# Kernel tuning notes

Hardware: AMD Instinct MI355X
Metric: run time of the kernel (lower is better)

The kernel has to match this reference:

```python
import jax, jax.numpy as jnp
import numpy as np


def maxpool2x2(x):
    # NCHW 2x2 max pool, stride 2
    return jax.lax.reduce_window(x, -jnp.inf, jax.lax.max, (1, 1, 2, 2), (1, 1, 2, 2), 'VALID')


def _xavier_uniform(k, shape):
    fan_out, fan_in = shape
    lim = np.sqrt(6.0 / (fan_in + fan_out))
    return jax.random.uniform(k, shape, jnp.float32, -lim, lim)


def setup_inputs() -> dict:
    key = jax.random.key(0)
    ks = jax.random.split(key, 5)
    C = 64
    x = jax.random.normal(ks[0], (4, C, 128, 128), jnp.float32)
    Wq = _xavier_uniform(ks[1], (C // 8, C))  # 1x1 conv == channel matmul
    Wk = _xavier_uniform(ks[2], (C // 8, C))
    Wv = _xavier_uniform(ks[3], (C // 2, C))
    Wo = _xavier_uniform(ks[4], (C, C // 2))
    gamma = jnp.full((1,), 0.1, jnp.float32)  # nonzero so attention branch contributes
    return {"x": x, "Wq": Wq, "Wk": Wk, "Wv": Wv, "Wo": Wo, "gamma": gamma}


def reference(x, Wq, Wk, Wv, Wo, gamma):
    b, c, w, h = x.shape
    # 1x1 convs as channel contractions
    q = jnp.einsum('oc,bchw->bohw', Wq, x).reshape(b, c // 8, w * h)          # [b, c/8, k]
    k_ = maxpool2x2(jnp.einsum('oc,bchw->bohw', Wk, x)).reshape(b, c // 8, -1)  # [b, c/8, f]
    v = maxpool2x2(jnp.einsum('oc,bchw->bohw', Wv, x)).reshape(b, c // 2, -1)   # [b, c/2, f]
    # softmax over full-resolution query positions k (last axis), per pooled position f
    weights = jax.nn.softmax(jnp.einsum('bcf,bck->bfk', k_, q), axis=-1)        # [b, f, k]
    out = jnp.einsum('bcf,bfk->bck', v, weights).reshape(b, c // 2, w, h)       # [b, c/2, w, h]
    out = jnp.einsum('oc,bchw->bohw', Wo, out)                                   # [b, c, w, h]
    return gamma * out + x
```

## Files before the change

### kernel.cpp

```cpp
#include <hip/hip_runtime.h>
#include <cstdint>
#include <cstddef>


#define LOG2E 1.44269504088896340736f

typedef __attribute__((ext_vector_type(8)))  __bf16 bf8_t;
typedef __attribute__((ext_vector_type(16))) float  fx16;

__device__ __forceinline__ unsigned short f2bf(float f) {
  unsigned int u = __builtin_bit_cast(unsigned int, f);
  u += 0x7FFFu + ((u >> 16) & 1u);
  return (unsigned short)(u >> 16);
}
__device__ __forceinline__ unsigned int pk2(unsigned short lo, unsigned short hi) {
  return (unsigned int)lo | ((unsigned int)hi << 16);
}
__device__ __forceinline__ int pi16(int s) {
  int m = (s >> 2) & 3;
  return (m == 1 || m == 2) ? (s ^ 12) : s;
}
__device__ __forceinline__ float max4(const float* a) {
  return fmaxf(fmaxf(a[0], a[1]), fmaxf(a[2], a[3]));
}

#if __has_builtin(__builtin_amdgcn_exp2f)
#define EXP2F __builtin_amdgcn_exp2f
#else
#define EXP2F exp2f
#endif

__global__ void __launch_bounds__(256) k_qkv(const float* __restrict__ x,
                                             const float* __restrict__ Wq,
                                             const float* __restrict__ Wk,
                                             const float* __restrict__ Wv,
                                             const float* __restrict__ Wo,
                                             unsigned short* __restrict__ Qp,
                                             unsigned short* __restrict__ KpB,
                                             float* __restrict__ Vp,
                                             unsigned short* __restrict__ Wop) {
  if (blockIdx.x == 256) {
    for (int i = threadIdx.x; i < 2048; i += 256) {
      int c = i & 31;
      Wop[i] = f2bf(Wo[(i & ~31) | (c & 16) | pi16(c & 15)]);
    }
    return;
  }
  __shared__ float ws[48][64];
  __shared__ float xs[16][256];
  int t = threadIdx.x;
  for (int i = t; i < 512; i += 256) {
    ws[i >> 6][i & 63] = Wq[i];
    ws[8 + (i >> 6)][i & 63] = Wk[i];
  }
  for (int i = t; i < 2048; i += 256) ws[16 + (i >> 6)][i & 63] = Wv[i];
  int b = blockIdx.x >> 6, frow = blockIdx.x & 63;
  int rg = t >> 6, fc = t & 63;
  const float* xb = x + (size_t)b * (64 * 16384) + frow * 256;
  float acc[12][4];
#pragma unroll
  for (int j = 0; j < 12; ++j)
#pragma unroll
    for (int p = 0; p < 4; ++p) acc[j][p] = 0.f;
  int cl = t >> 4, seg = t & 15;
  for (int cc = 0; cc < 4; ++cc) {
    __syncthreads();
    const float4* src =
        reinterpret_cast<const float4*>(xb + (size_t)(cc * 16 + cl) * 16384 + seg * 16);
    float4* dst = reinterpret_cast<float4*>(&xs[cl][seg * 16]);
#pragma unroll
    for (int j = 0; j < 4; ++j) dst[j] = src[j];
    __syncthreads();
#pragma unroll
    for (int c16 = 0; c16 < 16; ++c16) {
      int c = cc * 16 + c16;
      float2 xa = *reinterpret_cast<const float2*>(&xs[c16][2 * fc]);
      float2 xbv = *reinterpret_cast<const float2*>(&xs[c16][128 + 2 * fc]);
#pragma unroll
      for (int j = 0; j < 12; ++j) {
        float w = ws[12 * rg + j][c];
        acc[j][0] = fmaf(w, xa.x, acc[j][0]);
        acc[j][1] = fmaf(w, xa.y, acc[j][1]);
        acc[j][2] = fmaf(w, xbv.x, acc[j][2]);
        acc[j][3] = fmaf(w, xbv.y, acc[j][3]);
      }
    }
  }
  size_t idx = (size_t)b * 4096 + frow * 64 + fc;
  uint4 z4; z4.x = z4.y = z4.z = z4.w = 0u;
  if (rg == 0) {
#pragma unroll
    for (int p = 0; p < 4; ++p) {
      int kpos = frow * 256 + (p >> 1) * 128 + 2 * fc + (p & 1);
      uint4 qa;
      qa.x = pk2(f2bf(acc[0][p]), f2bf(acc[1][p]));
      qa.y = pk2(f2bf(acc[2][p]), f2bf(acc[3][p]));
      qa.z = pk2(f2bf(acc[4][p]), f2bf(acc[5][p]));
      qa.w = pk2(f2bf(acc[6][p]), f2bf(acc[7][p]));
      uint4* qdst = reinterpret_cast<uint4*>(Qp + ((size_t)b * 16384 + kpos) * 16);
      qdst[0] = qa; qdst[1] = z4;
    }
    uint2 kw;
    kw.x = pk2(f2bf(max4(acc[8]) * LOG2E), f2bf(max4(acc[9]) * LOG2E));
    kw.y = pk2(f2bf(max4(acc[10]) * LOG2E), f2bf(max4(acc[11]) * LOG2E));
    *reinterpret_cast<uint2*>(KpB + idx * 16) = kw;
  } else if (rg == 1) {
    uint2 kw;
    kw.x = pk2(f2bf(max4(acc[0]) * LOG2E), f2bf(max4(acc[1]) * LOG2E));
    kw.y = pk2(f2bf(max4(acc[2]) * LOG2E), f2bf(max4(acc[3]) * LOG2E));
    *reinterpret_cast<uint2*>(KpB + idx * 16 + 4) = kw;
    *reinterpret_cast<uint4*>(KpB + idx * 16 + 8) = z4;
    float* vd = Vp + idx * 32;
    *reinterpret_cast<float4*>(vd) =
        make_float4(max4(acc[4]), max4(acc[5]), max4(acc[6]), max4(acc[7]));
    *reinterpret_cast<float4*>(vd + 4) =
        make_float4(max4(acc[8]), max4(acc[9]), max4(acc[10]), max4(acc[11]));
  } else {
    float* vd = Vp + idx * 32 + (rg == 2 ? 8 : 20);
#pragma unroll
    for (int j4 = 0; j4 < 3; ++j4)
      *reinterpret_cast<float4*>(vd + 4 * j4) =
          make_float4(max4(acc[4 * j4]), max4(acc[4 * j4 + 1]),
                      max4(acc[4 * j4 + 2]), max4(acc[4 * j4 + 3]));
  }
}

__global__ void __launch_bounds__(1024) k_lsum(const unsigned short* __restrict__ Qp,
                                               const unsigned short* __restrict__ KpB,
                                               const float* __restrict__ Vp,
                                               unsigned short* __restrict__ Vpp) {
  int b = blockIdx.x >> 6, g = blockIdx.x & 63;
  int wv = threadIdx.x >> 6, lane = threadIdx.x & 63;
  int half = lane >> 5, l31 = lane & 31;
  const unsigned short* kb =
      KpB + ((size_t)(b * 4096 + g * 64 + l31)) * 16 + half * 8;
  bf8_t A0 = *reinterpret_cast<const bf8_t*>(kb);
  bf8_t A1 = *reinterpret_cast<const bf8_t*>(kb + 32 * 16);
  const unsigned short* qbase = Qp + ((size_t)b * 16384) * 16 + half * 8;
  fx16 z;
#pragma unroll
  for (int i = 0; i < 16; ++i) z[i] = 0.f;
  float l[32];
#pragma unroll
  for (int i = 0; i < 32; ++i) l[i] = 0.f;
  int t0 = wv * 32;
  bf8_t B = *reinterpret_cast<const bf8_t*>(qbase + (size_t)(t0 * 32 + l31) * 16);
  for (int i = 0; i < 32; ++i) {
    int tn = t0 + ((i + 1) & 31);
    bf8_t nB = *reinterpret_cast<const bf8_t*>(qbase + (size_t)(tn * 32 + l31) * 16);
    fx16 s0 = __builtin_amdgcn_mfma_f32_32x32x16_bf16(A0, B, z, 0, 0, 0);
    fx16 s1 = __builtin_amdgcn_mfma_f32_32x32x16_bf16(A1, B, z, 0, 0, 0);
#pragma unroll
    for (int r0 = 0; r0 < 16; ++r0) l[r0] += EXP2F(s0[r0]);
#pragma unroll
    for (int r0 = 0; r0 < 16; ++r0) l[16 + r0] += EXP2F(s1[r0]);
    B = nB;
  }
#pragma unroll
  for (int r0 = 0; r0 < 32; ++r0)
    for (int d = 1; d < 32; d <<= 1) l[r0] += __shfl_xor(l[r0], d);
  __shared__ float sl[16][2][32];
  __shared__ float Linv[64];
  __shared__ unsigned short Tv[32][72];
  if (l31 == 0) {
#pragma unroll
    for (int r0 = 0; r0 < 16; ++r0) {
      int row = (r0 & 3) + 8 * (r0 >> 2) + 4 * half;
      sl[wv][0][row] = l[r0];
      sl[wv][1][row] = l[16 + r0];
    }
  }
  __syncthreads();
  if (threadIdx.x < 64) {
    int fgi = threadIdx.x >> 5, row = threadIdx.x & 31;
    float L = 0.f;
#pragma unroll
    for (int w2 = 0; w2 < 16; ++w2) L += sl[w2][fgi][row];
    Linv[threadIdx.x] = 1.0f / L;
  }
  __syncthreads();
  if (threadIdx.x < 512) {
    int floc = threadIdx.x >> 3, c4 = (threadIdx.x & 7) * 4;
    float4 v = *reinterpret_cast<const float4*>(
        Vp + ((size_t)(b * 4096 + g * 64 + floc)) * 32 + c4);
    float s = Linv[floc];
    int dst = (floc & ~15) | pi16(floc & 15);
    Tv[c4][dst]     = f2bf(v.x * s);
    Tv[c4 + 1][dst] = f2bf(v.y * s);
    Tv[c4 + 2][dst] = f2bf(v.z * s);
    Tv[c4 + 3][dst] = f2bf(v.w * s);
  }
  __syncthreads();
  if (threadIdx.x < 256) {
    int c = threadIdx.x >> 3, u = threadIdx.x & 7;
    uint4 val = *reinterpret_cast<const uint4*>(&Tv[c][u * 8]);
    *reinterpret_cast<uint4*>(Vpp + ((size_t)(b * 32 + c)) * 4096 + g * 64 + u * 8) = val;
  }
}

__global__ void __launch_bounds__(512) k_attn(const unsigned short* __restrict__ Qp,
                                              const unsigned short* __restrict__ KpB,
                                              const unsigned short* __restrict__ Vpp,
                                              const unsigned short* __restrict__ Wop,
                                              const float* __restrict__ x,
                                              const float* __restrict__ gamma,
                                              float* __restrict__ out) {
  int b = blockIdx.x >> 8, kp = blockIdx.x & 255;
  int wv = threadIdx.x >> 6, lane = threadIdx.x & 63;
  int half = lane >> 5, l31 = lane & 31;
  int kbase = kp * 64;
  const unsigned short* qb = Qp + ((size_t)b * 16384 + kbase + l31) * 16 + half * 8;
  bf8_t Bq0 = *reinterpret_cast<const bf8_t*>(qb);
  bf8_t Bq1 = *reinterpret_cast<const bf8_t*>(qb + 32 * 16);
  fx16 z;
#pragma unroll
  for (int i = 0; i < 16; ++i) z[i] = 0.f;
  fx16 acc0 = z, acc1 = z;
  const unsigned short* kpB = KpB + ((size_t)b * 4096 + l31) * 16 + half * 8;
  const unsigned short* vpB = Vpp + ((size_t)(b * 32 + l31)) * 4096 + half * 8;
  int c0 = wv * 16;
  int f0 = c0 * 32;
  bf8_t Ak  = *reinterpret_cast<const bf8_t*>(kpB + (size_t)f0 * 16);
  bf8_t Av0 = *reinterpret_cast<const bf8_t*>(vpB + f0);
  bf8_t Av1 = *reinterpret_cast<const bf8_t*>(vpB + f0 + 16);
  for (int fc = 0; fc < 16; ++fc) {
    int f1 = (c0 + ((fc + 1) & 15)) * 32;
    bf8_t nAk  = *reinterpret_cast<const bf8_t*>(kpB + (size_t)f1 * 16);
    bf8_t nAv0 = *reinterpret_cast<const bf8_t*>(vpB + f1);
    bf8_t nAv1 = *reinterpret_cast<const bf8_t*>(vpB + f1 + 16);
    fx16 s0 = __builtin_amdgcn_mfma_f32_32x32x16_bf16(Ak, Bq0, z, 0, 0, 0);
    fx16 s1 = __builtin_amdgcn_mfma_f32_32x32x16_bf16(Ak, Bq1, z, 0, 0, 0);
    bf8_t P00, P01, P10, P11;
#pragma unroll
    for (int j = 0; j < 8; ++j) {
      P00[j] = (__bf16)EXP2F(s0[j]);
      P01[j] = (__bf16)EXP2F(s0[8 + j]);
    }
#pragma unroll
    for (int j = 0; j < 8; ++j) {
      P10[j] = (__bf16)EXP2F(s1[j]);
      P11[j] = (__bf16)EXP2F(s1[8 + j]);
    }
    acc0 = __builtin_amdgcn_mfma_f32_32x32x16_bf16(Av0, P00, acc0, 0, 0, 0);
    acc1 = __builtin_amdgcn_mfma_f32_32x32x16_bf16(Av0, P10, acc1, 0, 0, 0);
    acc0 = __builtin_amdgcn_mfma_f32_32x32x16_bf16(Av1, P01, acc0, 0, 0, 0);
    acc1 = __builtin_amdgcn_mfma_f32_32x32x16_bf16(Av1, P11, acc1, 0, 0, 0);
    Ak = nAk; Av0 = nAv0; Av1 = nAv1;
  }
  __shared__ float sacc[4][2][4][64][4];
  if (wv >= 4) {
    int s = wv - 4;
#pragma unroll
    for (int j4 = 0; j4 < 4; ++j4) {
      *reinterpret_cast<float4*>(&sacc[s][0][j4][lane][0]) =
          make_float4(acc0[4 * j4], acc0[4 * j4 + 1], acc0[4 * j4 + 2], acc0[4 * j4 + 3]);
      *reinterpret_cast<float4*>(&sacc[s][1][j4][lane][0]) =
          make_float4(acc1[4 * j4], acc1[4 * j4 + 1], acc1[4 * j4 + 2], acc1[4 * j4 + 3]);
    }
  }
  __syncthreads();
  if (wv < 4) {
#pragma unroll
    for (int j4 = 0; j4 < 4; ++j4) {
      float4 p0 = *reinterpret_cast<const float4*>(&sacc[wv][0][j4][lane][0]);
      float4 p1 = *reinterpret_cast<const float4*>(&sacc[wv][1][j4][lane][0]);
      p0.x += acc0[4 * j4]; p0.y += acc0[4 * j4 + 1];
      p0.z += acc0[4 * j4 + 2]; p0.w += acc0[4 * j4 + 3];
      p1.x += acc1[4 * j4]; p1.y += acc1[4 * j4 + 1];
      p1.z += acc1[4 * j4 + 2]; p1.w += acc1[4 * j4 + 3];
      *reinterpret_cast<float4*>(&sacc[wv][0][j4][lane][0]) = p0;
      *reinterpret_cast<float4*>(&sacc[wv][1][j4][lane][0]) = p1;
    }
  }
  __syncthreads();
  if (wv >= 4) return;
  int kt = wv & 1, ot = wv >> 1;
  fx16 tot;
#pragma unroll
  for (int j4 = 0; j4 < 4; ++j4) {
    float4 a0 = *reinterpret_cast<const float4*>(&sacc[0][kt][j4][lane][0]);
    float4 a1 = *reinterpret_cast<const float4*>(&sacc[1][kt][j4][lane][0]);
    float4 a2 = *reinterpret_cast<const float4*>(&sacc[2][kt][j4][lane][0]);
    float4 a3 = *reinterpret_cast<const float4*>(&sacc[3][kt][j4][lane][0]);
    tot[4 * j4]     = (a0.x + a1.x) + (a2.x + a3.x);
    tot[4 * j4 + 1] = (a0.y + a1.y) + (a2.y + a3.y);
    tot[4 * j4 + 2] = (a0.z + a1.z) + (a2.z + a3.z);
    tot[4 * j4 + 3] = (a0.w + a1.w) + (a2.w + a3.w);
  }
  bf8_t Ob0, Ob1;
#pragma unroll
  for (int j = 0; j < 8; ++j) { Ob0[j] = (__bf16)tot[j]; Ob1[j] = (__bf16)tot[8 + j]; }
  const unsigned short* wb = Wop + (ot * 32 + l31) * 32 + half * 8;
  bf8_t Aw0 = *reinterpret_cast<const bf8_t*>(wb);
  bf8_t Aw1 = *reinterpret_cast<const bf8_t*>(wb + 16);
  fx16 y = __builtin_amdgcn_mfma_f32_32x32x16_bf16(Aw0, Ob0, z, 0, 0, 0);
  y = __builtin_amdgcn_mfma_f32_32x32x16_bf16(Aw1, Ob1, y, 0, 0, 0);
  float g = gamma[0];
  int k = kbase + kt * 32 + l31;
  const float* xp = x + (size_t)b * 64 * 16384 + k;
  float* op = out + (size_t)b * 64 * 16384 + k;
#pragma unroll
  for (int r0 = 0; r0 < 16; ++r0) {
    int row = (r0 & 3) + 8 * (r0 >> 2) + 4 * half + ot * 32;
    op[(size_t)row * 16384] = fmaf(g, y[r0], xp[(size_t)row * 16384]);
  }
}

extern "C" void kernel_launch(void* const* d_in, const int* in_sizes, int n_in,
                              void* d_out, int out_size, void* d_ws, size_t ws_size,
                              hipStream_t stream) {
  const float* x     = (const float*)d_in[0];
  const float* Wq    = (const float*)d_in[1];
  const float* Wk    = (const float*)d_in[2];
  const float* Wv    = (const float*)d_in[3];
  const float* Wo    = (const float*)d_in[4];
  const float* gamma = (const float*)d_in[5];
  float* out = (float*)d_out;
  char* ws = (char*)d_ws;
  unsigned short* Qp  = (unsigned short*)(ws + 0);
  unsigned short* KpB = (unsigned short*)(ws + 2097152);
  float*          Vp  = (float*)(ws + 2621440);
  unsigned short* Vpp = (unsigned short*)(ws + 4718592);
  unsigned short* Wop = (unsigned short*)(ws + 5767168);

  k_qkv <<<dim3(257),  dim3(256),  0, stream>>>(x, Wq, Wk, Wv, Wo, Qp, KpB, Vp, Wop);
  k_lsum<<<dim3(256),  dim3(1024), 0, stream>>>(Qp, KpB, Vp, Vpp);
  k_attn<<<dim3(1024), dim3(512),  0, stream>>>(Qp, KpB, Vpp, Wop, x, gamma, out);
}
```

Before: 151.4 us.

## Restructure QKV projection kernel with 1024 threads, double-buffered x and shuffle pooling

The QKV projection kernel now runs 1024 threads per block, so each thread owns one pixel position and 12 output channels instead of four positions. Weights are read straight from global memory (uniform per wave, so they can use scalar loads) rather than staged in shared memory. The x tile is double-buffered so the next chunk loads while the current one is computed. The 2x2 max-pool now uses cross-lane shuffles, and only one lane in four writes K and V. This is meant to raise occupancy and overlap loads with compute in a kernel that has only 257 blocks, at the cost of more redundant weight loads and extra shuffle instructions.

```diff
diff --git a/kernel.cpp b/kernel.cpp
--- a/kernel.cpp
+++ b/kernel.cpp
@@ -20,8 +20,10 @@
   int m = (s >> 2) & 3;
   return (m == 1 || m == 2) ? (s ^ 12) : s;
 }
-__device__ __forceinline__ float max4(const float* a) {
-  return fmaxf(fmaxf(a[0], a[1]), fmaxf(a[2], a[3]));
+__device__ __forceinline__ float pool4(float v) {
+  v = fmaxf(v, __shfl_xor(v, 1));
+  v = fmaxf(v, __shfl_xor(v, 2));
+  return v;
 }
 
 #if __has_builtin(__builtin_amdgcn_exp2f)
@@ -30,98 +32,136 @@
 #define EXP2F exp2f
 #endif
 
-__global__ void __launch_bounds__(256) k_qkv(const float* __restrict__ x,
-                                             const float* __restrict__ Wq,
-                                             const float* __restrict__ Wk,
-                                             const float* __restrict__ Wv,
-                                             const float* __restrict__ Wo,
-                                             unsigned short* __restrict__ Qp,
-                                             unsigned short* __restrict__ KpB,
-                                             float* __restrict__ Vp,
-                                             unsigned short* __restrict__ Wop) {
+__global__ void __launch_bounds__(1024) k_qkv(const float* __restrict__ x,
+                                              const float* __restrict__ Wq,
+                                              const float* __restrict__ Wk,
+                                              const float* __restrict__ Wv,
+                                              const float* __restrict__ Wo,
+                                              unsigned short* __restrict__ Qp,
+                                              unsigned short* __restrict__ KpB,
+                                              float* __restrict__ Vp,
+                                              unsigned short* __restrict__ Wop) {
   if (blockIdx.x == 256) {
-    for (int i = threadIdx.x; i < 2048; i += 256) {
+    for (int i = threadIdx.x; i < 2048; i += 1024) {
       int c = i & 31;
       Wop[i] = f2bf(Wo[(i & ~31) | (c & 16) | pi16(c & 15)]);
     }
     return;
   }
-  __shared__ float ws[48][64];
-  __shared__ float xs[16][256];
+  __shared__ float xs[2][16][256];
   int t = threadIdx.x;
-  for (int i = t; i < 512; i += 256) {
-    ws[i >> 6][i & 63] = Wq[i];
-    ws[8 + (i >> 6)][i & 63] = Wk[i];
-  }
-  for (int i = t; i < 2048; i += 256) ws[16 + (i >> 6)][i & 63] = Wv[i];
   int b = blockIdx.x >> 6, frow = blockIdx.x & 63;
-  int rg = t >> 6, fc = t & 63;
+  int w = t >> 6, seg = t & 63;
+  int du = __builtin_amdgcn_readfirstlane(t >> 8);
+  int ph = t & 255, fl = ph >> 2, p = ph & 3;
+  int pos = ((ph & 2) << 6) | (fl << 1) | (ph & 1);
   const float* xb = x + (size_t)b * (64 * 16384) + frow * 256;
-  float acc[12][4];
-#pragma unroll
-  for (int j = 0; j < 12; ++j)
-#pragma unroll
-    for (int p = 0; p < 4; ++p) acc[j][p] = 0.f;
-  int cl = t >> 4, seg = t & 15;
+
+  const float* prow[12];
+  if (du == 0) {
+#pragma unroll
+    for (int j = 0; j < 8; ++j) prow[j] = Wq + j * 64;
+#pragma unroll
+    for (int j = 0; j < 4; ++j) prow[8 + j] = Wk + j * 64;
+  } else if (du == 1) {
+#pragma unroll
+    for (int j = 0; j < 4; ++j) prow[j] = Wk + (4 + j) * 64;
+#pragma unroll
+    for (int j = 0; j < 8; ++j) prow[4 + j] = Wv + j * 64;
+  } else if (du == 2) {
+#pragma unroll
+    for (int j = 0; j < 12; ++j) prow[j] = Wv + (8 + j) * 64;
+  } else {
+#pragma unroll
+    for (int j = 0; j < 12; ++j) prow[j] = Wv + (20 + j) * 64;
+  }
+
+  float acc[12];
+#pragma unroll
+  for (int j = 0; j < 12; ++j) acc[j] = 0.f;
+
+  {
+    float4 v = *reinterpret_cast<const float4*>(xb + (size_t)w * 16384 + seg * 4);
+    *reinterpret_cast<float4*>(&xs[0][w][seg * 4]) = v;
+  }
+  __syncthreads();
+
   for (int cc = 0; cc < 4; ++cc) {
+    int cur = cc & 1;
+    float4 nx;
+    if (cc < 3)
+      nx = *reinterpret_cast<const float4*>(
+          xb + (size_t)((cc + 1) * 16 + w) * 16384 + seg * 4);
+#pragma unroll
+    for (int c4 = 0; c4 < 4; ++c4) {
+      float4 wv[12];
+#pragma unroll
+      for (int j = 0; j < 12; ++j)
+        wv[j] = *reinterpret_cast<const float4*>(prow[j] + cc * 16 + c4 * 4);
+#pragma unroll
+      for (int u = 0; u < 4; ++u) {
+        float xv = xs[cur][c4 * 4 + u][pos];
+#pragma unroll
+        for (int j = 0; j < 12; ++j) {
+          float wj = reinterpret_cast<const float*>(&wv[j])[u];
+          acc[j] = fmaf(wj, xv, acc[j]);
+        }
+      }
+    }
     __syncthreads();
-    const float4* src =
-        reinterpret_cast<const float4*>(xb + (size_t)(cc * 16 + cl) * 16384 + seg * 16);
-    float4* dst = reinterpret_cast<float4*>(&xs[cl][seg * 16]);
-#pragma unroll
-    for (int j = 0; j < 4; ++j) dst[j] = src[j];
-    __syncthreads();
-#pragma unroll
-    for (int c16 = 0; c16 < 16; ++c16) {
-      int c = cc * 16 + c16;
-      float2 xa = *reinterpret_cast<const float2*>(&xs[c16][2 * fc]);
-      float2 xbv = *reinterpret_cast<const float2*>(&xs[c16][128 + 2 * fc]);
-#pragma unroll
-      for (int j = 0; j < 12; ++j) {
-        float w = ws[12 * rg + j][c];
-        acc[j][0] = fmaf(w, xa.x, acc[j][0]);
-        acc[j][1] = fmaf(w, xa.y, acc[j][1]);
-        acc[j][2] = fmaf(w, xbv.x, acc[j][2]);
-        acc[j][3] = fmaf(w, xbv.y, acc[j][3]);
-      }
-    }
-  }
-  size_t idx = (size_t)b * 4096 + frow * 64 + fc;
+    if (cc < 3) {
+      *reinterpret_cast<float4*>(&xs[cur ^ 1][w][seg * 4]) = nx;
+      __syncthreads();
+    }
+  }
+
+  size_t idx = (size_t)b * 4096 + frow * 64 + fl;
   uint4 z4; z4.x = z4.y = z4.z = z4.w = 0u;
-  if (rg == 0) {
-#pragma unroll
-    for (int p = 0; p < 4; ++p) {
-      int kpos = frow * 256 + (p >> 1) * 128 + 2 * fc + (p & 1);
-      uint4 qa;
-      qa.x = pk2(f2bf(acc[0][p]), f2bf(acc[1][p]));
-      qa.y = pk2(f2bf(acc[2][p]), f2bf(acc[3][p]));
-      qa.z = pk2(f2bf(acc[4][p]), f2bf(acc[5][p]));
-      qa.w = pk2(f2bf(acc[6][p]), f2bf(acc[7][p]));
-      uint4* qdst = reinterpret_cast<uint4*>(Qp + ((size_t)b * 16384 + kpos) * 16);
-      qdst[0] = qa; qdst[1] = z4;
-    }
-    uint2 kw;
-    kw.x = pk2(f2bf(max4(acc[8]) * LOG2E), f2bf(max4(acc[9]) * LOG2E));
-    kw.y = pk2(f2bf(max4(acc[10]) * LOG2E), f2bf(max4(acc[11]) * LOG2E));
-    *reinterpret_cast<uint2*>(KpB + idx * 16) = kw;
-  } else if (rg == 1) {
-    uint2 kw;
-    kw.x = pk2(f2bf(max4(acc[0]) * LOG2E), f2bf(max4(acc[1]) * LOG2E));
-    kw.y = pk2(f2bf(max4(acc[2]) * LOG2E), f2bf(max4(acc[3]) * LOG2E));
-    *reinterpret_cast<uint2*>(KpB + idx * 16 + 4) = kw;
-    *reinterpret_cast<uint4*>(KpB + idx * 16 + 8) = z4;
-    float* vd = Vp + idx * 32;
-    *reinterpret_cast<float4*>(vd) =
-        make_float4(max4(acc[4]), max4(acc[5]), max4(acc[6]), max4(acc[7]));
-    *reinterpret_cast<float4*>(vd + 4) =
-        make_float4(max4(acc[8]), max4(acc[9]), max4(acc[10]), max4(acc[11]));
+  if (du == 0) {
+    int kpos = frow * 256 + pos;
+    uint4 qa;
+    qa.x = pk2(f2bf(acc[0]), f2bf(acc[1]));
+    qa.y = pk2(f2bf(acc[2]), f2bf(acc[3]));
+    qa.z = pk2(f2bf(acc[4]), f2bf(acc[5]));
+    qa.w = pk2(f2bf(acc[6]), f2bf(acc[7]));
+    uint4* qdst = reinterpret_cast<uint4*>(Qp + ((size_t)b * 16384 + kpos) * 16);
+    qdst[0] = qa; qdst[1] = z4;
+    float m0 = pool4(acc[8]) * LOG2E, m1 = pool4(acc[9]) * LOG2E;
+    float m2 = pool4(acc[10]) * LOG2E, m3 = pool4(acc[11]) * LOG2E;
+    if (p == 0) {
+      uint2 kw;
+      kw.x = pk2(f2bf(m0), f2bf(m1));
+      kw.y = pk2(f2bf(m2), f2bf(m3));
+      *reinterpret_cast<uint2*>(KpB + idx * 16) = kw;
+    }
+  } else if (du == 1) {
+    float m0 = pool4(acc[0]) * LOG2E, m1 = pool4(acc[1]) * LOG2E;
+    float m2 = pool4(acc[2]) * LOG2E, m3 = pool4(acc[3]) * LOG2E;
+    float v0 = pool4(acc[4]), v1 = pool4(acc[5]);
+    float v2 = pool4(acc[6]), v3 = pool4(acc[7]);
+    float v4 = pool4(acc[8]), v5 = pool4(acc[9]);
+    float v6 = pool4(acc[10]), v7 = pool4(acc[11]);
+    if (p == 0) {
+      uint2 kw;
+      kw.x = pk2(f2bf(m0), f2bf(m1));
+      kw.y = pk2(f2bf(m2), f2bf(m3));
+      *reinterpret_cast<uint2*>(KpB + idx * 16 + 4) = kw;
+      *reinterpret_cast<uint4*>(KpB + idx * 16 + 8) = z4;
+      float* vd = Vp + idx * 32;
+      *reinterpret_cast<float4*>(vd) = make_float4(v0, v1, v2, v3);
+      *reinterpret_cast<float4*>(vd + 4) = make_float4(v4, v5, v6, v7);
+    }
   } else {
-    float* vd = Vp + idx * 32 + (rg == 2 ? 8 : 20);
-#pragma unroll
-    for (int j4 = 0; j4 < 3; ++j4)
-      *reinterpret_cast<float4*>(vd + 4 * j4) =
-          make_float4(max4(acc[4 * j4]), max4(acc[4 * j4 + 1]),
-                      max4(acc[4 * j4 + 2]), max4(acc[4 * j4 + 3]));
+    float m[12];
+#pragma unroll
+    for (int j = 0; j < 12; ++j) m[j] = pool4(acc[j]);
+    if (p == 0) {
+      float* vd = Vp + idx * 32 + (du == 2 ? 8 : 20);
+#pragma unroll
+      for (int j4 = 0; j4 < 3; ++j4)
+        *reinterpret_cast<float4*>(vd + 4 * j4) =
+            make_float4(m[4 * j4], m[4 * j4 + 1], m[4 * j4 + 2], m[4 * j4 + 3]);
+    }
   }
 }
 
@@ -323,7 +363,7 @@
   unsigned short* Vpp = (unsigned short*)(ws + 4718592);
   unsigned short* Wop = (unsigned short*)(ws + 5767168);
 
-  k_qkv <<<dim3(257),  dim3(256),  0, stream>>>(x, Wq, Wk, Wv, Wo, Qp, KpB, Vp, Wop);
+  k_qkv <<<dim3(257),  dim3(1024), 0, stream>>>(x, Wq, Wk, Wv, Wo, Qp, KpB, Vp, Wop);
   k_lsum<<<dim3(256),  dim3(1024), 0, stream>>>(Qp, KpB, Vp, Vpp);
   k_attn<<<dim3(1024), dim3(512),  0, stream>>>(Qp, KpB, Vpp, Wop, x, gamma, out);
 }
```

Result: no change. 152.1 us (+0.5%).
